# Kernel tuning notes

Measured on AMD Instinct MI355X. Metric: run time of the kernel, lower is better.

Reference implementation:

```python
import jax, jax.numpy as jnp
import numpy as np

H = 1024
N_IDX = 400000
NBINS = 256


def setup_inputs() -> dict:
    key = jax.random.key(0)
    ks = jax.random.split(key, 10)
    return {
        "input_data": jax.random.uniform(ks[0], (1, 3, H, H), jnp.float32),
        "target_data": jax.random.uniform(ks[1], (1, 3, H, H), jnp.float32) * 2.0 - 1.0,
        "ref": jax.random.uniform(ks[2], (1, 3, H, H), jnp.float32) * 2.0 - 1.0,
        "mask_src": (jax.random.uniform(ks[3], (1, 1, H, H)) > 0.3).astype(jnp.float32) * 255.0,
        "mask_tar": (jax.random.uniform(ks[4], (1, 1, H, H)) > 0.3).astype(jnp.float32) * 255.0,
        "target_data_eye": jax.random.uniform(ks[5], (1, 3, H, H), jnp.float32),
        "idx0": jax.random.randint(ks[6], (N_IDX,), 0, H),
        "idx1": jax.random.randint(ks[7], (N_IDX,), 0, H),
        "idx2": jax.random.randint(ks[8], (N_IDX,), 0, H),
        "idx3": jax.random.randint(ks[9], (N_IDX,), 0, H),
    }


def _cdf(vals):
    # vals: [3, N] float in [0, 256). torch.histc(bins=256, min=0, max=256) -> bin = floor(v)
    bins = jnp.clip(vals.astype(jnp.int32), 0, NBINS - 1)  # [3, N]
    hist = jnp.zeros((3, NBINS), jnp.float32).at[jnp.arange(3)[:, None], bins].add(1.0)
    cdf = jnp.cumsum(hist, axis=1)
    return cdf / cdf[:, -1:]  # normalized cumulative histogram, [3, 256]


def _trans_table(cdf_dst, cdf_ref):
    # cal_trans(ref=cdf_dst, adj=cdf_ref): table[i] = first j in [1,255]
    # with cdf_ref[j-1] <= cdf_dst[i] <= cdf_ref[j]; else table[i] = i; table[255] = 255
    r = cdf_dst[:, None]                  # [256, 1]
    lo = cdf_ref[None, :-1]               # [1, 255] -> adj[j-1], j = 1..255
    hi = cdf_ref[None, 1:]                # [1, 255] -> adj[j]
    cond = (r >= lo) & (r <= hi)          # [256, 255]
    has = cond.any(axis=1)
    j = jnp.argmax(cond, axis=1) + 1      # first matching j
    table = jnp.where(has, j, jnp.arange(NBINS))
    return table.at[NBINS - 1].set(NBINS - 1)


def _hist_match(dst_img, ref_img, i0, i1, i2, i3):
    # dst_img, ref_img: [3, H, W]; gather masked pixels per channel
    dst_align = dst_img[:, i0, i1]        # [3, N]
    ref_align = ref_img[:, i2, i3]        # [3, N]
    cdf_dst = _cdf(dst_align)
    cdf_ref = _cdf(ref_align)
    tables = jax.vmap(_trans_table)(cdf_dst, cdf_ref)  # [3, 256] int
    bins = jnp.clip(dst_align.astype(jnp.int32), 0, NBINS - 1)  # int() truncation, v >= 0
    matched = jnp.take_along_axis(tables, bins, axis=1).astype(dst_img.dtype)  # [3, N]
    return dst_img.at[:, i0, i1].set(matched)


def reference(input_data, target_data, ref, mask_src, mask_tar, target_data_eye,
              idx0, idx1, idx2, idx3):
    # part = 'lip' (generic part) -> histogram_matching branch; use_vgg = False
    de_norm = lambda x: jnp.clip((x + 1.0) / 2.0, 0.0, 1.0)
    target = (de_norm(target_data) * 255.0)[0]          # [3, H, W]
    inp = (jnp.clip(input_data, 0.0, 1.0) * 255.0)[0]   # [3, H, W]
    r = (de_norm(ref) * 255.0)[0]                       # [3, H, W]
    msrc = jnp.broadcast_to(mask_src / 255.0, (1, 3, H, H))[0]
    mtar = jnp.broadcast_to(mask_tar / 255.0, (1, 3, H, H))[0]

    input_masked = inp * msrc
    target_masked = target * mtar
    ref_masked = r * msrc

    input_match = jax.lax.stop_gradient(
        _hist_match(ref_masked, target_masked, idx0, idx1, idx2, idx3))

    loss = jnp.mean(jnp.abs(input_masked / 255.0 - input_match / 255.0))
    return ((target_masked / 255.0)[None], (ref_masked / 255.0)[None],
            (input_masked / 255.0)[None], (input_match / 255.0)[None], loss)
```

## Files before the change

### kernel.cpp

```cpp
#include <hip/hip_runtime.h>

#define H 1024
#define HH (H * H)
#define CHW (3 * HH)
#define NB 256

__device__ __forceinline__ float clamp01(float x) { return fminf(fmaxf(x, 0.0f), 1.0f); }

__device__ __forceinline__ unsigned int bin8(float v01) {
    int b = (int)(v01 * 255.0f);
    return (unsigned int)min(max(b, 0), NB - 1);
}

__global__ void k_elementwise(const float4* __restrict__ inp,
                              const float4* __restrict__ tar,
                              const float4* __restrict__ rfp,
                              const float4* __restrict__ msrc,
                              const float4* __restrict__ mtar,
                              float4* __restrict__ out0, float4* __restrict__ out1,
                              float4* __restrict__ out2, float4* __restrict__ out3,
                              uint4* __restrict__ pk_dst, uint4* __restrict__ pk_ref)
{
    int p = blockIdx.x * blockDim.x + threadIdx.x;
    if (p >= HH / 4) return;
    float4 ms4 = msrc[p], mt4 = mtar[p];
    float msx = ms4.x / 255.0f, msy = ms4.y / 255.0f, msz = ms4.z / 255.0f, msw = ms4.w / 255.0f;
    float mtx = mt4.x / 255.0f, mty = mt4.y / 255.0f, mtz = mt4.z / 255.0f, mtw = mt4.w / 255.0f;
    unsigned int bd0 = 0, bd1 = 0, bd2 = 0, bd3 = 0;
    unsigned int br0 = 0, br1 = 0, br2 = 0, br3 = 0;
#pragma unroll
    for (int c = 0; c < 3; ++c) {
        int q = c * (HH / 4) + p;
        float4 t = tar[q], r = rfp[q], iv = inp[q];
        float4 o0, o1, o2;
        o0.x = clamp01((t.x + 1.0f) * 0.5f) * mtx;
        o0.y = clamp01((t.y + 1.0f) * 0.5f) * mty;
        o0.z = clamp01((t.z + 1.0f) * 0.5f) * mtz;
        o0.w = clamp01((t.w + 1.0f) * 0.5f) * mtw;
        o1.x = clamp01((r.x + 1.0f) * 0.5f) * msx;
        o1.y = clamp01((r.y + 1.0f) * 0.5f) * msy;
        o1.z = clamp01((r.z + 1.0f) * 0.5f) * msz;
        o1.w = clamp01((r.w + 1.0f) * 0.5f) * msw;
        o2.x = clamp01(iv.x) * msx;
        o2.y = clamp01(iv.y) * msy;
        o2.z = clamp01(iv.z) * msz;
        o2.w = clamp01(iv.w) * msw;
        out0[q] = o0;
        out1[q] = o1;
        out3[q] = o1;
        out2[q] = o2;
        int sh = 8 * c;
        bd0 |= bin8(o1.x) << sh;  bd1 |= bin8(o1.y) << sh;
        bd2 |= bin8(o1.z) << sh;  bd3 |= bin8(o1.w) << sh;
        br0 |= bin8(o0.x) << sh;  br1 |= bin8(o0.y) << sh;
        br2 |= bin8(o0.z) << sh;  br3 |= bin8(o0.w) << sh;
    }
    pk_dst[p] = make_uint4(bd0, bd1, bd2, bd3);
    pk_ref[p] = make_uint4(br0, br1, br2, br3);
}

__global__ void k_hist(const unsigned int* __restrict__ pk_dst,
                       const unsigned int* __restrict__ pk_ref,
                       const int* __restrict__ i0, const int* __restrict__ i1,
                       const int* __restrict__ i2, const int* __restrict__ i3,
                       unsigned int* __restrict__ ghist, int n)
{
    __shared__ unsigned int h[2 * 3 * NB];
    for (int i = threadIdx.x; i < 2 * 3 * NB; i += blockDim.x) h[i] = 0u;
    __syncthreads();

    for (int k = blockIdx.x * blockDim.x + threadIdx.x; k < n; k += gridDim.x * blockDim.x) {
        int pd = i0[k] * H + i1[k];
        int pr = i2[k] * H + i3[k];
        unsigned int a = pk_dst[pd];
        unsigned int b = pk_ref[pr];
        atomicAdd(&h[        (a       & 255u)], 1u);
        atomicAdd(&h[  NB + ((a >> 8) & 255u)], 1u);
        atomicAdd(&h[2*NB + ((a >>16) & 255u)], 1u);
        atomicAdd(&h[3*NB + ( b       & 255u)], 1u);
        atomicAdd(&h[4*NB + ((b >> 8) & 255u)], 1u);
        atomicAdd(&h[5*NB + ((b >>16) & 255u)], 1u);
    }
    __syncthreads();
    for (int i = threadIdx.x; i < 2 * 3 * NB; i += blockDim.x) {
        unsigned int v = h[i];
        if (v) atomicAdd(&ghist[i], v);
    }
}

__global__ void k_tables(const uint4* __restrict__ ghist4, float* __restrict__ table)
{
    __shared__ float cdf[6][NB];
    int t = threadIdx.x;
    int wave = t >> 6, lane = t & 63;

    uint4 v = ghist4[wave * 64 + lane];
    unsigned int s0 = v.x;
    unsigned int s1 = s0 + v.y;
    unsigned int s2 = s1 + v.z;
    unsigned int s3 = s2 + v.w;

    unsigned int scan = s3;
#pragma unroll
    for (int off = 1; off < 64; off <<= 1) {
        unsigned int u = (unsigned int)__shfl_up((int)scan, off, 64);
        if (lane >= off) scan += u;
    }
    unsigned int prefix = scan - s3;
    unsigned int total  = (unsigned int)__shfl((int)scan, 63, 64);
    float ft = (float)total;

    cdf[wave][lane * 4 + 0] = (float)(prefix + s0) / ft;
    cdf[wave][lane * 4 + 1] = (float)(prefix + s1) / ft;
    cdf[wave][lane * 4 + 2] = (float)(prefix + s2) / ft;
    cdf[wave][lane * 4 + 3] = (float)(prefix + s3) / ft;
    __syncthreads();

    if (t < NB) {
#pragma unroll
        for (int c = 0; c < 3; ++c) {
            float r = cdf[c][t];
            const float* cr = cdf[3 + c];
            int lo = 1, hi = NB - 1;
#pragma unroll
            for (int it = 0; it < 8; ++it) {
                int mid = (lo + hi) >> 1;
                if (cr[mid] >= r) hi = mid; else lo = mid + 1;
            }
            int jstar = lo - 1;
            int tab = (jstar == 0 && cr[0] > r) ? t : (jstar + 1);
            if (t == NB - 1) tab = NB - 1;
            table[c * NB + t] = (float)tab / 255.0f;
        }
    }
}

__global__ void k_scatter(const unsigned int* __restrict__ pk_dst,
                          const int* __restrict__ i0, const int* __restrict__ i1,
                          const float* __restrict__ table, float* __restrict__ out3, int n)
{
    __shared__ float tl[3 * NB];
    for (int i = threadIdx.x; i < 3 * NB; i += blockDim.x) tl[i] = table[i];
    __syncthreads();
    int k = blockIdx.x * blockDim.x + threadIdx.x;
    if (k >= n) return;
    int pd = i0[k] * H + i1[k];
    unsigned int a = pk_dst[pd];
    out3[         pd] = tl[        (a       & 255u)];
    out3[HH     + pd] = tl[  NB + ((a >> 8) & 255u)];
    out3[2 * HH + pd] = tl[2*NB + ((a >>16) & 255u)];
}

__global__ void k_loss(const float4* __restrict__ a, const float4* __restrict__ b,
                       float* __restrict__ loss)
{
    float s = 0.0f;
    int n4 = CHW / 4;
    for (int i = blockIdx.x * blockDim.x + threadIdx.x; i < n4; i += gridDim.x * blockDim.x) {
        float4 x = a[i], y = b[i];
        s += fabsf(x.x - y.x) + fabsf(x.y - y.y) + fabsf(x.z - y.z) + fabsf(x.w - y.w);
    }
#pragma unroll
    for (int off = 32; off > 0; off >>= 1) s += __shfl_down(s, off);
    __shared__ float ws[4];
    int lane = threadIdx.x & 63, w = threadIdx.x >> 6;
    if (lane == 0) ws[w] = s;
    __syncthreads();
    if (threadIdx.x == 0) {
        float tsum = ws[0] + ws[1] + ws[2] + ws[3];
        atomicAdd(loss, tsum * (1.0f / (float)CHW));
    }
}

extern "C" void kernel_launch(void* const* d_in, const int* in_sizes, int n_in,
                              void* d_out, int out_size, void* d_ws, size_t ws_size,
                              hipStream_t stream)
{
    const float* inp  = (const float*)d_in[0];
    const float* tar  = (const float*)d_in[1];
    const float* rfp  = (const float*)d_in[2];
    const float* msrc = (const float*)d_in[3];
    const float* mtar = (const float*)d_in[4];
    const int* i0 = (const int*)d_in[6];
    const int* i1 = (const int*)d_in[7];
    const int* i2 = (const int*)d_in[8];
    const int* i3 = (const int*)d_in[9];
    int n = in_sizes[6];

    float* out0 = (float*)d_out;
    float* out1 = out0 + CHW;
    float* out2 = out1 + CHW;
    float* out3 = out2 + CHW;
    float* loss = out3 + CHW;

    unsigned int* ghist  = (unsigned int*)d_ws;
    float*        table  = (float*)((char*)d_ws + 6144);
    unsigned int* pk_dst = (unsigned int*)((char*)d_ws + 16384);
    unsigned int* pk_ref = pk_dst + HH;

    hipMemsetAsync(ghist, 0, 1536 * sizeof(unsigned int), stream);
    hipMemsetAsync(loss, 0, sizeof(float), stream);

    k_elementwise<<<(HH / 4 + 255) / 256, 256, 0, stream>>>(
        (const float4*)inp, (const float4*)tar, (const float4*)rfp,
        (const float4*)msrc, (const float4*)mtar,
        (float4*)out0, (float4*)out1, (float4*)out2, (float4*)out3,
        (uint4*)pk_dst, (uint4*)pk_ref);

    k_hist<<<784, 512, 0, stream>>>(pk_dst, pk_ref, i0, i1, i2, i3, ghist, n);

    k_tables<<<1, 384, 0, stream>>>((const uint4*)ghist, table);

    k_scatter<<<(n + 255) / 256, 256, 0, stream>>>(pk_dst, i0, i1, table, out3, n);

    k_loss<<<768, 256, 0, stream>>>((const float4*)out2, (const float4*)out3, loss);
}
```

Measured before the change: 192.5 us.

## Fuse table build into histogram via last-block pattern and drop memsets

Removes the two memset calls by zeroing the histogram, counter and loss inside block 0 of the elementwise kernel. Merges the table-building kernel into the histogram kernel: the last block to finish, found through an atomic counter, reads the global histogram and builds the transfer tables. Adds nontemporal stores for the out0 and out1 outputs, which are not read again. Together these cut launch overhead at the cost of a fence and atomic per block plus a serial tail in a single block.

```diff
diff --git a/kernel.cpp b/kernel.cpp
--- a/kernel.cpp
+++ b/kernel.cpp
@@ -4,12 +4,20 @@
 #define HH (H * H)
 #define CHW (3 * HH)
 #define NB 256
+#define HIST_BLOCKS 784
+
+typedef float nfloat4 __attribute__((ext_vector_type(4)));
 
 __device__ __forceinline__ float clamp01(float x) { return fminf(fmaxf(x, 0.0f), 1.0f); }
 
 __device__ __forceinline__ unsigned int bin8(float v01) {
     int b = (int)(v01 * 255.0f);
     return (unsigned int)min(max(b, 0), NB - 1);
+}
+
+__device__ __forceinline__ void nt_store4(float4 v, float4* p) {
+    nfloat4 nv; nv.x = v.x; nv.y = v.y; nv.z = v.z; nv.w = v.w;
+    __builtin_nontemporal_store(nv, reinterpret_cast<nfloat4*>(p));
 }
 
 __global__ void k_elementwise(const float4* __restrict__ inp,
@@ -19,8 +27,13 @@
                               const float4* __restrict__ mtar,
                               float4* __restrict__ out0, float4* __restrict__ out1,
                               float4* __restrict__ out2, float4* __restrict__ out3,
-                              uint4* __restrict__ pk_dst, uint4* __restrict__ pk_ref)
-{
+                              uint4* __restrict__ pk_dst, uint4* __restrict__ pk_ref,
+                              unsigned int* __restrict__ gz, float* __restrict__ loss)
+{
+    if (blockIdx.x == 0) {
+        for (int i = threadIdx.x; i < 1537; i += blockDim.x) gz[i] = 0u;
+        if (threadIdx.x == 0) *loss = 0.0f;
+    }
     int p = blockIdx.x * blockDim.x + threadIdx.x;
     if (p >= HH / 4) return;
     float4 ms4 = msrc[p], mt4 = mtar[p];
@@ -45,8 +58,8 @@
         o2.y = clamp01(iv.y) * msy;
         o2.z = clamp01(iv.z) * msz;
         o2.w = clamp01(iv.w) * msw;
-        out0[q] = o0;
-        out1[q] = o1;
+        nt_store4(o0, &out0[q]);
+        nt_store4(o1, &out1[q]);
         out3[q] = o1;
         out2[q] = o2;
         int sh = 8 * c;
@@ -63,9 +76,12 @@
                        const unsigned int* __restrict__ pk_ref,
                        const int* __restrict__ i0, const int* __restrict__ i1,
                        const int* __restrict__ i2, const int* __restrict__ i3,
-                       unsigned int* __restrict__ ghist, int n)
+                       unsigned int* __restrict__ ghist, unsigned int* __restrict__ counter,
+                       float* __restrict__ table, int n)
 {
     __shared__ unsigned int h[2 * 3 * NB];
+    __shared__ float cdf[6][NB];
+    __shared__ bool amLast;
     for (int i = threadIdx.x; i < 2 * 3 * NB; i += blockDim.x) h[i] = 0u;
     __syncthreads();
 
@@ -86,36 +102,39 @@
         unsigned int v = h[i];
         if (v) atomicAdd(&ghist[i], v);
     }
-}
-
-__global__ void k_tables(const uint4* __restrict__ ghist4, float* __restrict__ table)
-{
-    __shared__ float cdf[6][NB];
+
+    if (threadIdx.x == 0) {
+        __threadfence();
+        unsigned int old = atomicAdd(counter, 1u);
+        amLast = (old == (unsigned int)(gridDim.x - 1));
+    }
+    __syncthreads();
+    if (!amLast) return;
+
     int t = threadIdx.x;
-    int wave = t >> 6, lane = t & 63;
-
-    uint4 v = ghist4[wave * 64 + lane];
-    unsigned int s0 = v.x;
-    unsigned int s1 = s0 + v.y;
-    unsigned int s2 = s1 + v.z;
-    unsigned int s3 = s2 + v.w;
-
-    unsigned int scan = s3;
-#pragma unroll
-    for (int off = 1; off < 64; off <<= 1) {
-        unsigned int u = (unsigned int)__shfl_up((int)scan, off, 64);
-        if (lane >= off) scan += u;
-    }
-    unsigned int prefix = scan - s3;
-    unsigned int total  = (unsigned int)__shfl((int)scan, 63, 64);
-    float ft = (float)total;
-
-    cdf[wave][lane * 4 + 0] = (float)(prefix + s0) / ft;
-    cdf[wave][lane * 4 + 1] = (float)(prefix + s1) / ft;
-    cdf[wave][lane * 4 + 2] = (float)(prefix + s2) / ft;
-    cdf[wave][lane * 4 + 3] = (float)(prefix + s3) / ft;
-    __syncthreads();
-
+    if (t < 384) {
+        int wave = t >> 6, lane = t & 63;
+        int base = wave * NB + lane * 4;
+        unsigned int v0 = atomicAdd(&ghist[base + 0], 0u);
+        unsigned int v1 = atomicAdd(&ghist[base + 1], 0u);
+        unsigned int v2 = atomicAdd(&ghist[base + 2], 0u);
+        unsigned int v3 = atomicAdd(&ghist[base + 3], 0u);
+        unsigned int s0 = v0, s1 = s0 + v1, s2 = s1 + v2, s3 = s2 + v3;
+        unsigned int scan = s3;
+#pragma unroll
+        for (int off = 1; off < 64; off <<= 1) {
+            unsigned int u = (unsigned int)__shfl_up((int)scan, off, 64);
+            if (lane >= off) scan += u;
+        }
+        unsigned int prefix = scan - s3;
+        unsigned int total  = (unsigned int)__shfl((int)scan, 63, 64);
+        float ft = (float)total;
+        cdf[wave][lane * 4 + 0] = (float)(prefix + s0) / ft;
+        cdf[wave][lane * 4 + 1] = (float)(prefix + s1) / ft;
+        cdf[wave][lane * 4 + 2] = (float)(prefix + s2) / ft;
+        cdf[wave][lane * 4 + 3] = (float)(prefix + s3) / ft;
+    }
+    __syncthreads();
     if (t < NB) {
 #pragma unroll
         for (int c = 0; c < 3; ++c) {
@@ -193,23 +212,20 @@
     float* out3 = out2 + CHW;
     float* loss = out3 + CHW;
 
-    unsigned int* ghist  = (unsigned int*)d_ws;
-    float*        table  = (float*)((char*)d_ws + 6144);
-    unsigned int* pk_dst = (unsigned int*)((char*)d_ws + 16384);
-    unsigned int* pk_ref = pk_dst + HH;
-
-    hipMemsetAsync(ghist, 0, 1536 * sizeof(unsigned int), stream);
-    hipMemsetAsync(loss, 0, sizeof(float), stream);
+    unsigned int* ghist   = (unsigned int*)d_ws;
+    unsigned int* counter = ghist + 1536;
+    float*        table   = (float*)((char*)d_ws + 8192);
+    unsigned int* pk_dst  = (unsigned int*)((char*)d_ws + 16384);
+    unsigned int* pk_ref  = pk_dst + HH;
 
     k_elementwise<<<(HH / 4 + 255) / 256, 256, 0, stream>>>(
         (const float4*)inp, (const float4*)tar, (const float4*)rfp,
         (const float4*)msrc, (const float4*)mtar,
         (float4*)out0, (float4*)out1, (float4*)out2, (float4*)out3,
-        (uint4*)pk_dst, (uint4*)pk_ref);
-
-    k_hist<<<784, 512, 0, stream>>>(pk_dst, pk_ref, i0, i1, i2, i3, ghist, n);
-
-    k_tables<<<1, 384, 0, stream>>>((const uint4*)ghist, table);
+        (uint4*)pk_dst, (uint4*)pk_ref, ghist, loss);
+
+    k_hist<<<HIST_BLOCKS, 512, 0, stream>>>(pk_dst, pk_ref, i0, i1, i2, i3,
+                                            ghist, counter, table, n);
 
     k_scatter<<<(n + 255) / 256, 256, 0, stream>>>(pk_dst, i0, i1, table, out3, n);
 
```

Result: slower. 198.9 us (+3.3%).

## Fold memsets into elementwise kernel and ballot-aggregate zero-bin histogram atomics

Applied to the files above, without the earlier changes.

Removes the two hipMemsetAsync calls by zeroing the global histogram and loss from block 0 of the elementwise kernel, which saves two stream operations. In the histogram kernel, lanes whose packed value is zero (masked pixels, about 30% of samples) are counted with a wave ballot, and a single lane adds the popcount, which cuts contention on bin 0 of the shared-memory atomics. The histogram grid also shrinks from 784 to 768 blocks, and the table offset in the workspace moves.

```diff
diff --git a/kernel.cpp b/kernel.cpp
--- a/kernel.cpp
+++ b/kernel.cpp
@@ -4,6 +4,7 @@
 #define HH (H * H)
 #define CHW (3 * HH)
 #define NB 256
+#define HIST_BLOCKS 768
 
 __device__ __forceinline__ float clamp01(float x) { return fminf(fmaxf(x, 0.0f), 1.0f); }
 
@@ -19,8 +20,13 @@
                               const float4* __restrict__ mtar,
                               float4* __restrict__ out0, float4* __restrict__ out1,
                               float4* __restrict__ out2, float4* __restrict__ out3,
-                              uint4* __restrict__ pk_dst, uint4* __restrict__ pk_ref)
-{
+                              uint4* __restrict__ pk_dst, uint4* __restrict__ pk_ref,
+                              unsigned int* __restrict__ gz, float* __restrict__ loss)
+{
+    if (blockIdx.x == 0) {
+        for (int i = threadIdx.x; i < 1536; i += blockDim.x) gz[i] = 0u;
+        if (threadIdx.x == 0) *loss = 0.0f;
+    }
     int p = blockIdx.x * blockDim.x + threadIdx.x;
     if (p >= HH / 4) return;
     float4 ms4 = msrc[p], mt4 = mtar[p];
@@ -69,17 +75,36 @@
     for (int i = threadIdx.x; i < 2 * 3 * NB; i += blockDim.x) h[i] = 0u;
     __syncthreads();
 
+    int lane = threadIdx.x & 63;
     for (int k = blockIdx.x * blockDim.x + threadIdx.x; k < n; k += gridDim.x * blockDim.x) {
         int pd = i0[k] * H + i1[k];
         int pr = i2[k] * H + i3[k];
         unsigned int a = pk_dst[pd];
         unsigned int b = pk_ref[pr];
-        atomicAdd(&h[        (a       & 255u)], 1u);
-        atomicAdd(&h[  NB + ((a >> 8) & 255u)], 1u);
-        atomicAdd(&h[2*NB + ((a >>16) & 255u)], 1u);
-        atomicAdd(&h[3*NB + ( b       & 255u)], 1u);
-        atomicAdd(&h[4*NB + ((b >> 8) & 255u)], 1u);
-        atomicAdd(&h[5*NB + ((b >>16) & 255u)], 1u);
+
+        unsigned long long mza = __ballot(a == 0u);
+        if (a != 0u) {
+            atomicAdd(&h[        (a       & 255u)], 1u);
+            atomicAdd(&h[  NB + ((a >> 8) & 255u)], 1u);
+            atomicAdd(&h[2*NB + ((a >>16) & 255u)], 1u);
+        } else if (lane == __ffsll(mza) - 1) {
+            unsigned int cnt = (unsigned int)__popcll(mza);
+            atomicAdd(&h[0],      cnt);
+            atomicAdd(&h[NB],     cnt);
+            atomicAdd(&h[2 * NB], cnt);
+        }
+
+        unsigned long long mzb = __ballot(b == 0u);
+        if (b != 0u) {
+            atomicAdd(&h[3*NB + ( b       & 255u)], 1u);
+            atomicAdd(&h[4*NB + ((b >> 8) & 255u)], 1u);
+            atomicAdd(&h[5*NB + ((b >>16) & 255u)], 1u);
+        } else if (lane == __ffsll(mzb) - 1) {
+            unsigned int cnt = (unsigned int)__popcll(mzb);
+            atomicAdd(&h[3 * NB], cnt);
+            atomicAdd(&h[4 * NB], cnt);
+            atomicAdd(&h[5 * NB], cnt);
+        }
     }
     __syncthreads();
     for (int i = threadIdx.x; i < 2 * 3 * NB; i += blockDim.x) {
@@ -194,20 +219,17 @@
     float* loss = out3 + CHW;
 
     unsigned int* ghist  = (unsigned int*)d_ws;
-    float*        table  = (float*)((char*)d_ws + 6144);
+    float*        table  = (float*)((char*)d_ws + 8192);
     unsigned int* pk_dst = (unsigned int*)((char*)d_ws + 16384);
     unsigned int* pk_ref = pk_dst + HH;
-
-    hipMemsetAsync(ghist, 0, 1536 * sizeof(unsigned int), stream);
-    hipMemsetAsync(loss, 0, sizeof(float), stream);
 
     k_elementwise<<<(HH / 4 + 255) / 256, 256, 0, stream>>>(
         (const float4*)inp, (const float4*)tar, (const float4*)rfp,
         (const float4*)msrc, (const float4*)mtar,
         (float4*)out0, (float4*)out1, (float4*)out2, (float4*)out3,
-        (uint4*)pk_dst, (uint4*)pk_ref);
-
-    k_hist<<<784, 512, 0, stream>>>(pk_dst, pk_ref, i0, i1, i2, i3, ghist, n);
+        (uint4*)pk_dst, (uint4*)pk_ref, ghist, loss);
+
+    k_hist<<<HIST_BLOCKS, 512, 0, stream>>>(pk_dst, pk_ref, i0, i1, i2, i3, ghist, n);
 
     k_tables<<<1, 384, 0, stream>>>((const uint4*)ghist, table);
 
```

Result: faster. 188.0 us (-2.3%).
